# Kernel optimization log

Hardware: AMD Instinct MI355X
Metric: run time of the kernel (lower is better)

Reference implementation:

```python
import jax, jax.numpy as jnp
import numpy as np


def setup_inputs() -> dict:
    key = jax.random.key(0)
    k1, k2 = jax.random.split(key)
    B, T, D = 16, 1024, 256
    z = jax.random.normal(k1, (B, T, D), dtype=jnp.float32)
    gt_dT = jax.random.normal(k2, (B, T, T, 4), dtype=jnp.float32)
    sigma = jnp.full((4,), 0.1, dtype=jnp.float32)
    return {"z": z, "gt_dT": gt_dT, "sigma": sigma}


def reference(z, gt_dT, sigma):
    # z: [B,T,D], gt_dT: [B,T,T,4], sigma: [4]
    B, T, D = z.shape
    # Gaussian kernel over pairwise displacements -> w: [B,T,T]
    inv2s2 = 1.0 / (2.0 * sigma * sigma)  # [4]
    kernel = jnp.einsum('btsk,k->bts', gt_dT * gt_dT, inv2s2)
    w = jnp.exp(-kernel)  # [B,T,T]

    z2 = jnp.sum(z * z, axis=-1)          # [B,T]
    w_col_sum = jnp.sum(w, axis=2)        # [B,T]
    term1 = jnp.sum(z2 * w_col_sum, axis=1)  # [B]

    wz = jnp.einsum('bts,bsd->btd', w, z)    # [B,T,D]
    term2 = jnp.sum(wz * z, axis=(1, 2))     # [B]

    w_row_sum = jnp.sum(w, axis=1)           # [B,T]
    term3 = jnp.sum(z2 * w_row_sum, axis=1)  # [B]

    loss = jnp.mean(term1 - 2.0 * term2 + term3) / (T * T)
    return loss
```

## Files before the change

kernel.cpp:

```cpp
#include <hip/hip_runtime.h>
#include <hip/hip_bf16.h>
#include <stdint.h>

#define BB 16
#define TT 1024
#define DD 256

typedef __attribute__((ext_vector_type(8))) short short8;
typedef __attribute__((ext_vector_type(4))) float floatx4;

__device__ __forceinline__ unsigned short f2bf(float f) {
    union { float f; unsigned int u; } c; c.f = f;
    unsigned int u = c.u;
    unsigned int r = (u + 0x7FFFu + ((u >> 16) & 1u)) >> 16;
    return (unsigned short)r;
}

__global__ __launch_bounds__(256) void prep_kernel(
    const float* __restrict__ z, float* __restrict__ z2,
    unsigned short* __restrict__ zb, double* __restrict__ acc) {
    if (blockIdx.x == 0 && threadIdx.x == 0) *acc = 0.0;
    const int lane = threadIdx.x & 63;
    const int row  = blockIdx.x * 4 + (threadIdx.x >> 6);
    const float4 v = ((const float4*)(z + (size_t)row * DD))[lane];
    float ss = v.x * v.x + v.y * v.y + v.z * v.z + v.w * v.w;
    ushort4 o;
    o.x = f2bf(v.x); o.y = f2bf(v.y); o.z = f2bf(v.z); o.w = f2bf(v.w);
    ((ushort4*)(zb + (size_t)row * DD))[lane] = o;
#pragma unroll
    for (int off = 32; off > 0; off >>= 1) ss += __shfl_down(ss, off);
    if (lane == 0) z2[row] = ss;
}

__global__ __launch_bounds__(256) void patch_kernel(
    const unsigned short* __restrict__ zb, const float* __restrict__ z2,
    const float* __restrict__ gt, const float* __restrict__ sigma,
    double* __restrict__ acc) {
    const float LOG2E = 1.4426950408889634f;
    const float s0v = sigma[0], s1v = sigma[1], s2v = sigma[2], s3v = sigma[3];
    const float c0 = LOG2E * 0.5f / (s0v * s0v);
    const float c1 = LOG2E * 0.5f / (s1v * s1v);
    const float c2 = LOG2E * 0.5f / (s2v * s2v);
    const float c3 = LOG2E * 0.5f / (s3v * s3v);

    const int tid  = threadIdx.x;
    const int lane = tid & 63;
    const int quad = lane >> 4;
    const int m    = lane & 15;
    const int wid  = blockIdx.x * 4 + (tid >> 6);
    const int nW   = gridDim.x * 4;
    const int nTiles = BB * (TT / 32) * (TT / 32);

    float partial = 0.f;

    for (int tile = wid; tile < nTiles; tile += nW) {
        const int b   = tile >> 10;
        const int rem = tile & 1023;
        const int t0  = (rem >> 5) << 5;
        const int s0  = (rem & 31) << 5;

        const unsigned short* zrow = zb + (size_t)b * TT * DD;
        const short8* at0 = (const short8*)(zrow + (t0 + m) * DD + quad * 8);
        const short8* at1 = (const short8*)(zrow + (t0 + 16 + m) * DD + quad * 8);
        const short8* bs0 = (const short8*)(zrow + (s0 + m) * DD + quad * 8);
        const short8* bs1 = (const short8*)(zrow + (s0 + 16 + m) * DD + quad * 8);

        floatx4 g00 = {0.f, 0.f, 0.f, 0.f};
        floatx4 g01 = {0.f, 0.f, 0.f, 0.f};
        floatx4 g10 = {0.f, 0.f, 0.f, 0.f};
        floatx4 g11 = {0.f, 0.f, 0.f, 0.f};
#pragma unroll
        for (int k = 0; k < 8; ++k) {
            const short8 a0 = at0[k * 4];
            const short8 a1 = at1[k * 4];
            const short8 b0 = bs0[k * 4];
            const short8 b1 = bs1[k * 4];
            g00 = __builtin_amdgcn_mfma_f32_16x16x32_bf16(a0, b0, g00, 0, 0, 0);
            g01 = __builtin_amdgcn_mfma_f32_16x16x32_bf16(a0, b1, g01, 0, 0, 0);
            g10 = __builtin_amdgcn_mfma_f32_16x16x32_bf16(a1, b0, g10, 0, 0, 0);
            g11 = __builtin_amdgcn_mfma_f32_16x16x32_bf16(a1, b1, g11, 0, 0, 0);
        }

        const float* z2b  = z2 + b * TT;
        const float  z2s0 = z2b[s0 + m];
        const float  z2s1 = z2b[s0 + 16 + m];
        const float* gtb  = gt + (size_t)b * TT * TT * 4;
        const int    tq   = t0 + quad * 4;

#pragma unroll
        for (int r = 0; r < 4; ++r) {
            const float z2t0 = z2b[tq + r];
            const float z2t1 = z2b[tq + 16 + r];
            {
                const float4 d = *(const float4*)(gtb + ((size_t)(tq + r) * TT + (s0 + m)) * 4);
                const float kern = c0 * d.x * d.x + c1 * d.y * d.y + c2 * d.z * d.z + c3 * d.w * d.w;
                partial += exp2f(-kern) * (z2t0 + z2s0 - 2.f * g00[r]);
            }
            {
                const float4 d = *(const float4*)(gtb + ((size_t)(tq + r) * TT + (s0 + 16 + m)) * 4);
                const float kern = c0 * d.x * d.x + c1 * d.y * d.y + c2 * d.z * d.z + c3 * d.w * d.w;
                partial += exp2f(-kern) * (z2t0 + z2s1 - 2.f * g01[r]);
            }
            {
                const float4 d = *(const float4*)(gtb + ((size_t)(tq + 16 + r) * TT + (s0 + m)) * 4);
                const float kern = c0 * d.x * d.x + c1 * d.y * d.y + c2 * d.z * d.z + c3 * d.w * d.w;
                partial += exp2f(-kern) * (z2t1 + z2s0 - 2.f * g10[r]);
            }
            {
                const float4 d = *(const float4*)(gtb + ((size_t)(tq + 16 + r) * TT + (s0 + 16 + m)) * 4);
                const float kern = c0 * d.x * d.x + c1 * d.y * d.y + c2 * d.z * d.z + c3 * d.w * d.w;
                partial += exp2f(-kern) * (z2t1 + z2s1 - 2.f * g11[r]);
            }
        }
    }

#pragma unroll
    for (int off = 32; off > 0; off >>= 1) partial += __shfl_down(partial, off);
    __shared__ float red[4];
    if (lane == 0) red[tid >> 6] = partial;
    __syncthreads();
    if (tid == 0) atomicAdd(acc, (double)(red[0] + red[1] + red[2] + red[3]));
}

__global__ void finalize_kernel(const double* __restrict__ acc, float* __restrict__ out) {
    out[0] = (float)(*acc * (1.0 / ((double)BB * (double)TT * (double)TT)));
}

extern "C" void kernel_launch(void* const* d_in, const int* in_sizes, int n_in,
                              void* d_out, int out_size, void* d_ws, size_t ws_size,
                              hipStream_t stream) {
    const float* z     = (const float*)d_in[0];
    const float* gt    = (const float*)d_in[1];
    const float* sigma = (const float*)d_in[2];
    float* out = (float*)d_out;

    char* ws = (char*)d_ws;
    double* acc        = (double*)ws;
    float* z2          = (float*)(ws + 64);
    unsigned short* zb = (unsigned short*)(ws + 64 + (size_t)BB * TT * sizeof(float));

    prep_kernel<<<BB * TT / 4, 256, 0, stream>>>(z, z2, zb, acc);
    patch_kernel<<<2048, 256, 0, stream>>>(zb, z2, gt, sigma, acc);
    finalize_kernel<<<1, 1, 0, stream>>>(acc, out);
}
```

Before: 402.3 us.

## Assign one tile per wave and prefetch gt_dT before the MFMA loop

```diff
diff --git a/kernel.cpp b/kernel.cpp
--- a/kernel.cpp
+++ b/kernel.cpp
@@ -38,79 +38,92 @@
     double* __restrict__ acc) {
     const float LOG2E = 1.4426950408889634f;
     const float s0v = sigma[0], s1v = sigma[1], s2v = sigma[2], s3v = sigma[3];
-    const float c0 = LOG2E * 0.5f / (s0v * s0v);
-    const float c1 = LOG2E * 0.5f / (s1v * s1v);
-    const float c2 = LOG2E * 0.5f / (s2v * s2v);
-    const float c3 = LOG2E * 0.5f / (s3v * s3v);
+    const float nc0 = -LOG2E * 0.5f / (s0v * s0v);
+    const float nc1 = -LOG2E * 0.5f / (s1v * s1v);
+    const float nc2 = -LOG2E * 0.5f / (s2v * s2v);
+    const float nc3 = -LOG2E * 0.5f / (s3v * s3v);
 
     const int tid  = threadIdx.x;
     const int lane = tid & 63;
     const int quad = lane >> 4;
     const int m    = lane & 15;
     const int wid  = blockIdx.x * 4 + (tid >> 6);
-    const int nW   = gridDim.x * 4;
-    const int nTiles = BB * (TT / 32) * (TT / 32);
+
+    const int b   = wid >> 10;
+    const int rem = wid & 1023;
+    const int t0  = (rem >> 5) << 5;
+    const int s0  = (rem & 31) << 5;
+
+    const float* gtb = gt + (size_t)b * TT * TT * 4;
+    const int    tq  = t0 + quad * 4;
+
+    float4 gtv[16];
+#pragma unroll
+    for (int r = 0; r < 4; ++r) {
+        const size_t row0 = (size_t)(tq + r) * TT;
+        const size_t row1 = (size_t)(tq + 16 + r) * TT;
+        gtv[r * 4 + 0] = *(const float4*)(gtb + (row0 + (s0 + m)) * 4);
+        gtv[r * 4 + 1] = *(const float4*)(gtb + (row0 + (s0 + 16 + m)) * 4);
+        gtv[r * 4 + 2] = *(const float4*)(gtb + (row1 + (s0 + m)) * 4);
+        gtv[r * 4 + 3] = *(const float4*)(gtb + (row1 + (s0 + 16 + m)) * 4);
+    }
+
+    const unsigned short* zrow = zb + (size_t)b * TT * DD;
+    const short8* at0 = (const short8*)(zrow + (t0 + m) * DD + quad * 8);
+    const short8* at1 = (const short8*)(zrow + (t0 + 16 + m) * DD + quad * 8);
+    const short8* bs0 = (const short8*)(zrow + (s0 + m) * DD + quad * 8);
+    const short8* bs1 = (const short8*)(zrow + (s0 + 16 + m) * DD + quad * 8);
+
+    floatx4 g00 = {0.f, 0.f, 0.f, 0.f};
+    floatx4 g01 = {0.f, 0.f, 0.f, 0.f};
+    floatx4 g10 = {0.f, 0.f, 0.f, 0.f};
+    floatx4 g11 = {0.f, 0.f, 0.f, 0.f};
+#pragma unroll
+    for (int k = 0; k < 8; ++k) {
+        const short8 a0 = at0[k * 4];
+        const short8 a1 = at1[k * 4];
+        const short8 b0 = bs0[k * 4];
+        const short8 b1 = bs1[k * 4];
+        g00 = __builtin_amdgcn_mfma_f32_16x16x32_bf16(a0, b0, g00, 0, 0, 0);
+        g01 = __builtin_amdgcn_mfma_f32_16x16x32_bf16(a0, b1, g01, 0, 0, 0);
+        g10 = __builtin_amdgcn_mfma_f32_16x16x32_bf16(a1, b0, g10, 0, 0, 0);
+        g11 = __builtin_amdgcn_mfma_f32_16x16x32_bf16(a1, b1, g11, 0, 0, 0);
+    }
+
+    const float* z2b  = z2 + b * TT;
+    const float  z2s0 = z2b[s0 + m];
+    const float  z2s1 = z2b[s0 + 16 + m];
 
     float partial = 0.f;
-
-    for (int tile = wid; tile < nTiles; tile += nW) {
-        const int b   = tile >> 10;
-        const int rem = tile & 1023;
-        const int t0  = (rem >> 5) << 5;
-        const int s0  = (rem & 31) << 5;
-
-        const unsigned short* zrow = zb + (size_t)b * TT * DD;
-        const short8* at0 = (const short8*)(zrow + (t0 + m) * DD + quad * 8);
-        const short8* at1 = (const short8*)(zrow + (t0 + 16 + m) * DD + quad * 8);
-        const short8* bs0 = (const short8*)(zrow + (s0 + m) * DD + quad * 8);
-        const short8* bs1 = (const short8*)(zrow + (s0 + 16 + m) * DD + quad * 8);
-
-        floatx4 g00 = {0.f, 0.f, 0.f, 0.f};
-        floatx4 g01 = {0.f, 0.f, 0.f, 0.f};
-        floatx4 g10 = {0.f, 0.f, 0.f, 0.f};
-        floatx4 g11 = {0.f, 0.f, 0.f, 0.f};
 #pragma unroll
-        for (int k = 0; k < 8; ++k) {
-            const short8 a0 = at0[k * 4];
-            const short8 a1 = at1[k * 4];
-            const short8 b0 = bs0[k * 4];
-            const short8 b1 = bs1[k * 4];
-            g00 = __builtin_amdgcn_mfma_f32_16x16x32_bf16(a0, b0, g00, 0, 0, 0);
-            g01 = __builtin_amdgcn_mfma_f32_16x16x32_bf16(a0, b1, g01, 0, 0, 0);
-            g10 = __builtin_amdgcn_mfma_f32_16x16x32_bf16(a1, b0, g10, 0, 0, 0);
-            g11 = __builtin_amdgcn_mfma_f32_16x16x32_bf16(a1, b1, g11, 0, 0, 0);
+    for (int r = 0; r < 4; ++r) {
+        const float z2t0 = z2b[tq + r];
+        const float z2t1 = z2b[tq + 16 + r];
+        const float e00 = z2t0 + z2s0, e01 = z2t0 + z2s1;
+        const float e10 = z2t1 + z2s0, e11 = z2t1 + z2s1;
+        {
+            const float4 d = gtv[r * 4 + 0];
+            const float k2 = fmaf(nc3, d.w * d.w, fmaf(nc2, d.z * d.z,
+                             fmaf(nc1, d.y * d.y, nc0 * d.x * d.x)));
+            partial = fmaf(exp2f(k2), fmaf(-2.f, g00[r], e00), partial);
         }
-
-        const float* z2b  = z2 + b * TT;
-        const float  z2s0 = z2b[s0 + m];
-        const float  z2s1 = z2b[s0 + 16 + m];
-        const float* gtb  = gt + (size_t)b * TT * TT * 4;
-        const int    tq   = t0 + quad * 4;
-
-#pragma unroll
-        for (int r = 0; r < 4; ++r) {
-            const float z2t0 = z2b[tq + r];
-            const float z2t1 = z2b[tq + 16 + r];
-            {
-                const float4 d = *(const float4*)(gtb + ((size_t)(tq + r) * TT + (s0 + m)) * 4);
-                const float kern = c0 * d.x * d.x + c1 * d.y * d.y + c2 * d.z * d.z + c3 * d.w * d.w;
-                partial += exp2f(-kern) * (z2t0 + z2s0 - 2.f * g00[r]);
-            }
-            {
-                const float4 d = *(const float4*)(gtb + ((size_t)(tq + r) * TT + (s0 + 16 + m)) * 4);
-                const float kern = c0 * d.x * d.x + c1 * d.y * d.y + c2 * d.z * d.z + c3 * d.w * d.w;
-                partial += exp2f(-kern) * (z2t0 + z2s1 - 2.f * g01[r]);
-            }
-            {
-                const float4 d = *(const float4*)(gtb + ((size_t)(tq + 16 + r) * TT + (s0 + m)) * 4);
-                const float kern = c0 * d.x * d.x + c1 * d.y * d.y + c2 * d.z * d.z + c3 * d.w * d.w;
-                partial += exp2f(-kern) * (z2t1 + z2s0 - 2.f * g10[r]);
-            }
-            {
-                const float4 d = *(const float4*)(gtb + ((size_t)(tq + 16 + r) * TT + (s0 + 16 + m)) * 4);
-                const float kern = c0 * d.x * d.x + c1 * d.y * d.y + c2 * d.z * d.z + c3 * d.w * d.w;
-                partial += exp2f(-kern) * (z2t1 + z2s1 - 2.f * g11[r]);
-            }
+        {
+            const float4 d = gtv[r * 4 + 1];
+            const float k2 = fmaf(nc3, d.w * d.w, fmaf(nc2, d.z * d.z,
+                             fmaf(nc1, d.y * d.y, nc0 * d.x * d.x)));
+            partial = fmaf(exp2f(k2), fmaf(-2.f, g01[r], e01), partial);
+        }
+        {
+            const float4 d = gtv[r * 4 + 2];
+            const float k2 = fmaf(nc3, d.w * d.w, fmaf(nc2, d.z * d.z,
+                             fmaf(nc1, d.y * d.y, nc0 * d.x * d.x)));
+            partial = fmaf(exp2f(k2), fmaf(-2.f, g10[r], e10), partial);
+        }
+        {
+            const float4 d = gtv[r * 4 + 3];
+            const float k2 = fmaf(nc3, d.w * d.w, fmaf(nc2, d.z * d.z,
+                             fmaf(nc1, d.y * d.y, nc0 * d.x * d.x)));
+            partial = fmaf(exp2f(k2), fmaf(-2.f, g11[r], e11), partial);
         }
     }
 
@@ -140,6 +153,6 @@
     unsigned short* zb = (unsigned short*)(ws + 64 + (size_t)BB * TT * sizeof(float));
 
     prep_kernel<<<BB * TT / 4, 256, 0, stream>>>(z, z2, zb, acc);
-    patch_kernel<<<2048, 256, 0, stream>>>(zb, z2, gt, sigma, acc);
+    patch_kernel<<<BB * (TT / 32) * (TT / 32) / 4, 256, 0, stream>>>(zb, z2, gt, sigma, acc);
     finalize_kernel<<<1, 1, 0, stream>>>(acc, out);
 }
```

Result: no change. 402.4 us (+0.0%).
